# Performance work log

Hardware: AMD Instinct MI355X
Metric: run time of the kernel (lower is better)

## Reference

```python
import jax, jax.numpy as jnp
import numpy as np
import itertools, math

B, T, D = 4, 4096, 1024
H = 16
DIM = D // H          # 64
L, KB = 8, 4
R = 1 << KB           # 16
S = L * R             # 128
TOPK = 2


def setup_inputs() -> dict:
    key = jax.random.key(0)
    ks = jax.random.split(key, 8)
    x = jax.random.normal(ks[0], (B, T, D), dtype=jnp.float32)
    mask = jnp.ones((B, T), dtype=jnp.float32)
    sc = 1.0 / math.sqrt(D)
    Wq = jax.random.normal(ks[1], (D, D), dtype=jnp.float32) * sc
    Wk = jax.random.normal(ks[2], (D, D), dtype=jnp.float32) * sc
    Wv = jax.random.normal(ks[3], (D, D), dtype=jnp.float32) * sc
    Wout = jax.random.normal(ks[4], (D, D), dtype=jnp.float32) * sc
    b_out = jnp.zeros((D,), dtype=jnp.float32)
    # planes: (L, K_bits, head_dim) -> stored transposed as (head_dim, L*K_bits)
    planes = jax.random.normal(ks[5], (L * KB, DIM), dtype=jnp.float32)
    planes_T = planes.T
    # hypercube corners (R, K_bits) -> stored transposed as (K_bits, R)
    corners = jnp.asarray(list(itertools.product([-1.0, 1.0], repeat=KB)), dtype=jnp.float32)
    protos_T = corners.T
    logit_temp = jnp.zeros((), dtype=jnp.float32)  # log(1.0)
    return {"x": x, "mask": mask, "Wq": Wq, "Wk": Wk, "Wv": Wv,
            "Wout": Wout, "b_out": b_out, "planes_T": planes_T,
            "protos_T": protos_T, "logit_temp": logit_temp}


def reference(x, mask, Wq, Wk, Wv, Wout, b_out, planes_T, protos_T, logit_temp):
    b, t, d = x.shape
    Q = (x @ Wq).reshape(b, t, H, DIM)
    K = (x @ Wk).reshape(b, t, H, DIM)
    V = (x @ Wv).reshape(b, t, H, DIM)
    m = mask[:, :, None, None]
    Q, K, V = Q * m, K * m, V * m
    Q = jnp.transpose(Q, (0, 2, 1, 3))  # [B,H,T,dim]
    K = jnp.transpose(K, (0, 2, 1, 3))
    V = jnp.transpose(V, (0, 2, 1, 3))

    scale = jnp.clip(jnp.exp(logit_temp), 0.01, 20.0)
    # LSH hyperplane projections of K
    projK = jnp.einsum('bhtd,dp->bhtp', K, planes_T).reshape(b, H, t, L, KB)
    logitsK = jnp.einsum('bhtlk,kr->bhtlr', jnp.tanh(projK) / scale, protos_T)
    probsK = jax.nn.softmax(logitsK, axis=-1)  # [B,H,T,L,R]

    # top-k mask over R, then renormalize
    _, top_idx = jax.lax.top_k(probsK, TOPK)
    sel = jax.nn.one_hot(top_idx, R, dtype=probsK.dtype).sum(axis=-2)
    probsK = probsK * sel
    probsK = probsK / (probsK.sum(axis=-1, keepdims=True) + 1e-6)

    assign = probsK.reshape(b, H, t, S)  # [B,H,T,S]
    bucket_K = jnp.einsum('bhts,bhtd->bhsd', assign, K)
    bucket_V = jnp.einsum('bhts,bhtd->bhsd', assign, V)
    A = assign.sum(axis=2)[..., None]  # [B,H,S,1]
    bucket_K = bucket_K / (A + 1e-6)
    bucket_V = bucket_V / (A + 1e-6)

    scores = jnp.einsum('bhtd,bhsd->bhts', Q, bucket_K) / math.sqrt(DIM)
    probs_attn = jax.nn.softmax(scores, axis=-1)
    out = jnp.einsum('bhts,bhsd->bhtd', probs_attn, bucket_V)
    out = jnp.transpose(out, (0, 2, 1, 3)).reshape(b, t, d)
    return out @ Wout + b_out
```

## Files before the change

kernel.cpp:

```cpp
#include <hip/hip_runtime.h>
#include <math.h>
#include <stdint.h>

#define TT   4096
#define DD   1024
#define HH   16
#define DIMM 64
#define SS   128

typedef short bf16x8 __attribute__((ext_vector_type(8)));
typedef float f32x4  __attribute__((ext_vector_type(4)));

__device__ __forceinline__ unsigned short f2bf(float f) {
    uint32_t u = __float_as_uint(f);
    return (unsigned short)((u + 0x7fffu + ((u >> 16) & 1u)) >> 16);
}
__device__ __forceinline__ float bf2f(unsigned short h) {
    return __uint_as_float((uint32_t)h << 16);
}

#define GLD16(ldsp, gp) __builtin_amdgcn_global_load_lds( \
    (const __attribute__((address_space(1))) uint32_t*)(gp), \
    (__attribute__((address_space(3))) uint32_t*)(ldsp), 16, 0, 0)

__global__ __launch_bounds__(256) void cvt2_k(const float* __restrict__ x,
                                              unsigned short* __restrict__ xb,
                                              unsigned short* __restrict__ xlo)
{
    const size_t i = ((size_t)blockIdx.x * 256 + threadIdx.x) * 8;
    const float4 a = *(const float4*)&x[i];
    const float4 b = *(const float4*)&x[i + 4];
    const float v[8] = {a.x, a.y, a.z, a.w, b.x, b.y, b.z, b.w};
    unsigned short h[8], l[8];
#pragma unroll
    for (int j = 0; j < 8; j++) {
        h[j] = f2bf(v[j]);
        l[j] = f2bf(v[j] - bf2f(h[j]));
    }
    uint4 rh, rl;
    rh.x = (uint32_t)h[0] | ((uint32_t)h[1] << 16);
    rh.y = (uint32_t)h[2] | ((uint32_t)h[3] << 16);
    rh.z = (uint32_t)h[4] | ((uint32_t)h[5] << 16);
    rh.w = (uint32_t)h[6] | ((uint32_t)h[7] << 16);
    rl.x = (uint32_t)l[0] | ((uint32_t)l[1] << 16);
    rl.y = (uint32_t)l[2] | ((uint32_t)l[3] << 16);
    rl.z = (uint32_t)l[4] | ((uint32_t)l[5] << 16);
    rl.w = (uint32_t)l[6] | ((uint32_t)l[7] << 16);
    *(uint4*)&xb[i]  = rh;
    *(uint4*)&xlo[i] = rl;
}

__global__ __launch_bounds__(256) void tr_k(const float* __restrict__ W,
                                            unsigned short* __restrict__ WT)
{
    __shared__ unsigned short tile[32][33];
    const int bx = blockIdx.x * 32;
    const int by = blockIdx.y * 32;
    const int tx = threadIdx.x & 31, ty = threadIdx.x >> 5;
#pragma unroll
    for (int r = 0; r < 4; r++) {
        const int row = by + ty * 4 + r;
        tile[tx][ty * 4 + r] = f2bf(W[(size_t)row * 1024 + bx + tx]);
    }
    __syncthreads();
#pragma unroll
    for (int r = 0; r < 4; r++) {
        const int col = bx + ty * 4 + r;
        WT[(size_t)col * 1024 + by + tx] = tile[ty * 4 + r][tx];
    }
}

__global__ __launch_bounds__(256) void tr2_k(const float* __restrict__ Wp,
                                             unsigned short* __restrict__ WphT,
                                             unsigned short* __restrict__ WplT)
{
    __shared__ float tile[32][33];
    const int bx = blockIdx.x * 32;
    const int by = blockIdx.y * 32;
    const int tx = threadIdx.x & 31, ty = threadIdx.x >> 5;
#pragma unroll
    for (int r = 0; r < 4; r++) {
        const int row = by + ty * 4 + r;
        tile[tx][ty * 4 + r] = Wp[(size_t)row * 512 + bx + tx];
    }
    __syncthreads();
#pragma unroll
    for (int r = 0; r < 4; r++) {
        const int col = bx + ty * 4 + r;
        const float v = tile[ty * 4 + r][tx];
        const unsigned short hi = f2bf(v);
        const unsigned short lo = f2bf(v - bf2f(hi));
        WphT[(size_t)col * 1024 + by + tx] = hi;
        WplT[(size_t)col * 1024 + by + tx] = lo;
    }
}

template<int MODE>
__global__ __launch_bounds__(256) void mgemm_k(
    const unsigned short* __restrict__ Abf, const unsigned short* __restrict__ BT,
    const float* __restrict__ aux, float* __restrict__ C)
{
    __shared__ short sA[4096];
    __shared__ short sB[4096];
    const int tid = threadIdx.x;
    const int w  = tid >> 6;
    const int ln = tid & 63;
    const int wm = w & 1, wn = w >> 1;
    const int row0 = blockIdx.y * 128;
    const int col0 = blockIdx.x * 128;
    const int lr = ln >> 4, lc = ln & 15;

    f32x4 acc[4][4];
#pragma unroll
    for (int i = 0; i < 4; i++)
#pragma unroll
        for (int j = 0; j < 4; j++) acc[i][j] = (f32x4){0.f, 0.f, 0.f, 0.f};

    const int ia0 = 2 * w, ia1 = 2 * w + 1;
    const size_t gA0 = (size_t)(row0 + ia0 * 16 + lc) * 1024 + lr * 8;
    const size_t gA1 = (size_t)(row0 + ia1 * 16 + lc) * 1024 + lr * 8;
    const size_t gB0 = (size_t)(col0 + ia0 * 16 + lc) * 1024 + lr * 8;
    const size_t gB1 = (size_t)(col0 + ia1 * 16 + lc) * 1024 + lr * 8;

    for (int k0 = 0; k0 < 1024; k0 += 32) {
        GLD16(&sA[ia0 * 512], Abf + gA0 + k0);
        GLD16(&sA[ia1 * 512], Abf + gA1 + k0);
        GLD16(&sB[ia0 * 512], BT  + gB0 + k0);
        GLD16(&sB[ia1 * 512], BT  + gB1 + k0);
        __syncthreads();

        bf16x8 af[4], bfr[4];
#pragma unroll
        for (int ib = 0; ib < 4; ib++)
            af[ib] = *(const bf16x8*)&sA[(wm * 4 + ib) * 512 + ln * 8];
#pragma unroll
        for (int jb = 0; jb < 4; jb++)
            bfr[jb] = *(const bf16x8*)&sB[(wn * 4 + jb) * 512 + ln * 8];
#pragma unroll
        for (int ib = 0; ib < 4; ib++)
#pragma unroll
            for (int jb = 0; jb < 4; jb++)
                acc[ib][jb] = __builtin_amdgcn_mfma_f32_16x16x32_bf16(
                    af[ib], bfr[jb], acc[ib][jb], 0, 0, 0);
        __syncthreads();
    }

    if (MODE == 0) {
        const int h = col0 / 64 + wn;
#pragma unroll
        for (int ib = 0; ib < 4; ib++) {
#pragma unroll
            for (int r = 0; r < 4; r++) {
                const int gr = row0 + wm * 64 + ib * 16 + lr * 4 + r;
                const float mval = aux[gr];
                const int b = gr >> 12, t = gr & (TT - 1);
                float* base = C + (((size_t)(b * HH + h) * TT + t) * DIMM);
#pragma unroll
                for (int jb = 0; jb < 4; jb++)
                    base[jb * 16 + lc] = acc[ib][jb][r] * mval;
            }
        }
    } else if (MODE == 1) {
#pragma unroll
        for (int ib = 0; ib < 4; ib++) {
#pragma unroll
            for (int r = 0; r < 4; r++) {
                const int gr = row0 + wm * 64 + ib * 16 + lr * 4 + r;
#pragma unroll
                for (int jb = 0; jb < 4; jb++) {
                    const int col = col0 + wn * 64 + jb * 16 + lc;
                    C[(size_t)gr * 1024 + col] = acc[ib][jb][r] + aux[col];
                }
            }
        }
    } else {
        const int h = col0 / 64 + wn;
        unsigned short* Qf = (unsigned short*)C;
#pragma unroll
        for (int ib = 0; ib < 4; ib++) {
#pragma unroll
            for (int r = 0; r < 4; r++) {
                const int gr = row0 + wm * 64 + ib * 16 + lr * 4 + r;
                const float mval = aux[gr];
                const int b = gr >> 12;
                const int tt = gr & 127;
                const size_t tbase = (size_t)(b * HH + h) * 262144
                                   + (size_t)((gr & (TT - 1)) >> 7) * 8192;
#pragma unroll
                for (int jb = 0; jb < 4; jb++) {
                    const int d = jb * 16 + lc;
                    const int e = ((tt >> 4) * 2 + (d >> 5)) * 512 +
                                  ((tt & 15) + ((d >> 3) & 3) * 16) * 8 + (d & 7);
                    Qf[tbase + e] = f2bf(acc[ib][jb][r] * mval);
                }
            }
        }
    }
}

__global__ __launch_bounds__(256) void projm_k(
    const unsigned short* __restrict__ Ah, const unsigned short* __restrict__ Al,
    const unsigned short* __restrict__ Bh, const unsigned short* __restrict__ Bl,
    const float* __restrict__ mask, float* __restrict__ P)
{
    __shared__ short sAh[4096];
    __shared__ short sAl[4096];
    __shared__ short sBh[4096];
    __shared__ short sBl[4096];
    const int tid = threadIdx.x;
    const int w  = tid >> 6;
    const int ln = tid & 63;
    const int wm = w & 1, wn = w >> 1;
    const int row0 = blockIdx.y * 128;
    const int col0 = blockIdx.x * 128;
    const int lr = ln >> 4, lc = ln & 15;

    f32x4 acc[4][4];
#pragma unroll
    for (int i = 0; i < 4; i++)
#pragma unroll
        for (int j = 0; j < 4; j++) acc[i][j] = (f32x4){0.f, 0.f, 0.f, 0.f};

    const int ia0 = 2 * w, ia1 = 2 * w + 1;
    const size_t gA0 = (size_t)(row0 + ia0 * 16 + lc) * 1024 + lr * 8;
    const size_t gA1 = (size_t)(row0 + ia1 * 16 + lc) * 1024 + lr * 8;
    const size_t gB0 = (size_t)(col0 + ia0 * 16 + lc) * 1024 + lr * 8;
    const size_t gB1 = (size_t)(col0 + ia1 * 16 + lc) * 1024 + lr * 8;

    for (int k0 = 0; k0 < 1024; k0 += 32) {
        GLD16(&sAh[ia0 * 512], Ah + gA0 + k0);
        GLD16(&sAh[ia1 * 512], Ah + gA1 + k0);
        GLD16(&sAl[ia0 * 512], Al + gA0 + k0);
        GLD16(&sAl[ia1 * 512], Al + gA1 + k0);
        GLD16(&sBh[ia0 * 512], Bh + gB0 + k0);
        GLD16(&sBh[ia1 * 512], Bh + gB1 + k0);
        GLD16(&sBl[ia0 * 512], Bl + gB0 + k0);
        GLD16(&sBl[ia1 * 512], Bl + gB1 + k0);
        __syncthreads();

        bf16x8 ah[4], al[4], bh[4], bl[4];
#pragma unroll
        for (int ib = 0; ib < 4; ib++) {
            ah[ib] = *(const bf16x8*)&sAh[(wm * 4 + ib) * 512 + ln * 8];
            al[ib] = *(const bf16x8*)&sAl[(wm * 4 + ib) * 512 + ln * 8];
        }
#pragma unroll
        for (int jb = 0; jb < 4; jb++) {
            bh[jb] = *(const bf16x8*)&sBh[(wn * 4 + jb) * 512 + ln * 8];
            bl[jb] = *(const bf16x8*)&sBl[(wn * 4 + jb) * 512 + ln * 8];
        }
#pragma unroll
        for (int ib = 0; ib < 4; ib++)
#pragma unroll
            for (int jb = 0; jb < 4; jb++) {
                acc[ib][jb] = __builtin_amdgcn_mfma_f32_16x16x32_bf16(
                    ah[ib], bh[jb], acc[ib][jb], 0, 0, 0);
                acc[ib][jb] = __builtin_amdgcn_mfma_f32_16x16x32_bf16(
                    ah[ib], bl[jb], acc[ib][jb], 0, 0, 0);
                acc[ib][jb] = __builtin_amdgcn_mfma_f32_16x16x32_bf16(
                    al[ib], bh[jb], acc[ib][jb], 0, 0, 0);
            }
        __syncthreads();
    }

#pragma unroll
    for (int ib = 0; ib < 4; ib++) {
#pragma unroll
        for (int r = 0; r < 4; r++) {
            const int gr = row0 + wm * 64 + ib * 16 + lr * 4 + r;
            const float mval = mask[gr];
            const int b = gr >> 12, t = gr & (TT - 1);
#pragma unroll
            for (int jb = 0; jb < 4; jb++) {
                const int c = col0 + wn * 64 + jb * 16 + lc;
                const int h = c >> 5, p = c & 31;
                P[(((size_t)(b * HH + h) * TT + t) * 32) + p] =
                    acc[ib][jb][r] * mval;
            }
        }
    }
}

__global__ __launch_bounds__(256) void wproj_k(
    const float* __restrict__ Wk, const float* __restrict__ planesT,
    float* __restrict__ Wp)
{
    __shared__ float sW[1024];
    __shared__ float sP[2048];
    const int tid = threadIdx.x;
    const int k = blockIdx.x;
    for (int i = tid; i < 1024; i += 256) sW[i] = Wk[(size_t)k * 1024 + i];
    for (int i = tid; i < 2048; i += 256) sP[i] = planesT[i];
    __syncthreads();
#pragma unroll
    for (int c0 = 0; c0 < 2; c0++) {
        const int c = c0 * 256 + tid;
        const int h = c >> 5, p = c & 31;
        float s = 0.f;
#pragma unroll
        for (int d = 0; d < 64; d++)
            s = fmaf(sW[h * 64 + d], sP[d * 32 + p], s);
        Wp[(size_t)k * 512 + c] = s;
    }
}

__global__ __launch_bounds__(256) void zero_k(float* __restrict__ p)
{
    const size_t i = ((size_t)blockIdx.x * 256 + threadIdx.x) * 4;
    *(float4*)&p[i] = make_float4(0.f, 0.f, 0.f, 0.f);
}

__global__ __launch_bounds__(256) void assign_k(
    const float* __restrict__ Pj, const float* __restrict__ protosT,
    const float* __restrict__ logit_temp,
    unsigned char* __restrict__ aIdx, float* __restrict__ aW,
    float* __restrict__ gA)
{
    __shared__ float sPr[4][16];
    __shared__ float sCnt[SS];
    const int tid = threadIdx.x;
    const int tc = blockIdx.x;
    const int bh = blockIdx.y;

    if (tid < 64)  ((float*)sPr)[tid] = protosT[tid];
    if (tid < SS)  sCnt[tid] = 0.f;
    __syncthreads();

    const float scale = fminf(fmaxf(__expf(logit_temp[0]), 0.01f), 20.0f);
    const float inv_scale = 1.0f / scale;

    const int t = tc * 256 + tid;
    const float* pr = Pj + ((size_t)bh * TT + t) * 32;
    float proj[32];
#pragma unroll
    for (int j = 0; j < 8; j++) {
        const float4 v = *(const float4*)&pr[j * 4];
        proj[j * 4 + 0] = v.x; proj[j * 4 + 1] = v.y;
        proj[j * 4 + 2] = v.z; proj[j * 4 + 3] = v.w;
    }
#pragma unroll
    for (int p = 0; p < 32; p++) proj[p] = tanhf(proj[p]) * inv_scale;

    unsigned char idx[16];
    float wv[16];
#pragma unroll
    for (int l = 0; l < 8; l++) {
        float g[16];
#pragma unroll
        for (int r = 0; r < 16; r++)
            g[r] = proj[l * 4 + 0] * sPr[0][r] + proj[l * 4 + 1] * sPr[1][r] +
                   proj[l * 4 + 2] * sPr[2][r] + proj[l * 4 + 3] * sPr[3][r];
        float mx = g[0];
#pragma unroll
        for (int r = 1; r < 16; r++) mx = fmaxf(mx, g[r]);
        float Zs = 0.f;
#pragma unroll
        for (int r = 0; r < 16; r++) Zs += __expf(g[r] - mx);
        int a = 0; float ga = g[0];
#pragma unroll
        for (int r = 1; r < 16; r++) { if (g[r] > ga) { ga = g[r]; a = r; } }
        int b2 = (a == 0) ? 1 : 0; float gb = g[b2];
#pragma unroll
        for (int r = 0; r < 16; r++) { if (r != a && g[r] > gb) { gb = g[r]; b2 = r; } }
        const float pa = __expf(ga - mx) / Zs;
        const float pb = __expf(gb - mx) / Zs;
        const float den = pa + pb + 1e-6f;
        const float wa = pa / den, wb = pb / den;
        idx[l * 2 + 0] = (unsigned char)(l * 16 + a);  wv[l * 2 + 0] = wa;
        idx[l * 2 + 1] = (unsigned char)(l * 16 + b2); wv[l * 2 + 1] = wb;
        atomicAdd(&sCnt[l * 16 + a],  wa);
        atomicAdd(&sCnt[l * 16 + b2], wb);
    }
    const size_t off = (size_t)bh * TT + t;
    uint32_t pk[4];
#pragma unroll
    for (int j = 0; j < 4; j++)
        pk[j] = (uint32_t)idx[j * 4] | ((uint32_t)idx[j * 4 + 1] << 8) |
                ((uint32_t)idx[j * 4 + 2] << 16) | ((uint32_t)idx[j * 4 + 3] << 24);
    *(uint4*)&aIdx[off * 16] = make_uint4(pk[0], pk[1], pk[2], pk[3]);
#pragma unroll
    for (int j = 0; j < 4; j++)
        *(float4*)&aW[off * 16 + j * 4] =
            make_float4(wv[j * 4], wv[j * 4 + 1], wv[j * 4 + 2], wv[j * 4 + 3]);
    __syncthreads();
    if (tid < SS) atomicAdd(&gA[bh * SS + tid], sCnt[tid]);
}

__global__ __launch_bounds__(256) void scatter4_k(
    const float* __restrict__ Kb, const float* __restrict__ Vb,
    const unsigned char* __restrict__ aIdx, const float* __restrict__ aW,
    float* __restrict__ gBK, float* __restrict__ gBV)
{
    __shared__ short sA[8192];
    __shared__ short sB[8192];
    const int tid = threadIdx.x;
    const int tc = blockIdx.x;
    const int bh = blockIdx.y;
    const int w  = tid >> 6, ln = tid & 63;
    const int wm = w & 1, wn = w >> 1;

    f32x4 acc[4][4];
#pragma unroll
    for (int i = 0; i < 4; i++)
#pragma unroll
        for (int j = 0; j < 4; j++) acc[i][j] = (f32x4){0.f, 0.f, 0.f, 0.f};

    const int scol = tid & 127;
    const int stg  = tid >> 7;
    const float* srcrow = (scol < 64)
        ? Kb + (size_t)bh * (TT * DIMM) + scol
        : Vb + (size_t)bh * (TT * DIMM) + (scol - 64);
    const int bchunk = (scol >> 4);
    const int bslot8 = (scol & 15) * 8;
    const int ptt = tid >> 2, pg = tid & 3;

    for (int c = 0; c < 8; c++) {
        const int t0 = tc * 512 + c * 64;
        __syncthreads();
        {
            const uint4 z = make_uint4(0u, 0u, 0u, 0u);
#pragma unroll
            for (int r = 0; r < 4; r++)
                *(uint4*)&sA[(r * 256 + tid) * 8] = z;
        }
        __syncthreads();
#pragma unroll 8
        for (int r = 0; r < 32; r++) {
            const int tt = stg * 32 + r;
            const float v = srcrow[(size_t)(t0 + tt) * DIMM];
            sB[((tt >> 5) * 8 + bchunk) * 512 + ((tt >> 3) & 3) * 128 +
               bslot8 + (tt & 7)] = f2bf(v);
        }
        {
            const size_t off = (size_t)bh * TT + (t0 + ptt);
            const uint32_t pk = ((const uint32_t*)aIdx)[off * 4 + pg];
            const float4 wv = *(const float4*)&aW[off * 16 + pg * 4];
            const float w4[4] = {wv.x, wv.y, wv.z, wv.w};
#pragma unroll
            for (int q = 0; q < 4; q++) {
                const int s = (pk >> (8 * q)) & 255;
                sA[((ptt >> 5) * 8 + (s >> 4)) * 512 + ((ptt >> 3) & 3) * 128 +
                   (s & 15) * 8 + (ptt & 7)] = f2bf(w4[q]);
            }
        }
        __syncthreads();
#pragma unroll
        for (int ks = 0; ks < 2; ks++) {
            bf16x8 af[4], bfr[4];
#pragma unroll
            for (int ib = 0; ib < 4; ib++)
                af[ib] = *(const bf16x8*)&sA[(ks * 8 + wm * 4 + ib) * 512 + ln * 8];
#pragma unroll
            for (int jb = 0; jb < 4; jb++)
                bfr[jb] = *(const bf16x8*)&sB[(ks * 8 + wn * 4 + jb) * 512 + ln * 8];
#pragma unroll
            for (int ib = 0; ib < 4; ib++)
#pragma unroll
                for (int jb = 0; jb < 4; jb++)
                    acc[ib][jb] = __builtin_amdgcn_mfma_f32_16x16x32_bf16(
                        af[ib], bfr[jb], acc[ib][jb], 0, 0, 0);
        }
    }

    const int lr = ln >> 4, lc = ln & 15;
#pragma unroll
    for (int ib = 0; ib < 4; ib++) {
#pragma unroll
        for (int r = 0; r < 4; r++) {
            const int s = wm * 64 + ib * 16 + lr * 4 + r;
#pragma unroll
            for (int jb = 0; jb < 4; jb++) {
                const int col = wn * 64 + jb * 16 + lc;
                if (col < 64)
                    atomicAdd(&gBK[(size_t)bh * (SS * DIMM) + s * DIMM + col],
                              acc[ib][jb][r]);
                else
                    atomicAdd(&gBV[(size_t)bh * (SS * DIMM) + s * DIMM + (col - 64)],
                              acc[ib][jb][r]);
            }
        }
    }
}

__global__ __launch_bounds__(256) void bprep_k(
    const float* __restrict__ gBK, const float* __restrict__ gBV,
    const float* __restrict__ gA,
    unsigned short* __restrict__ Kf, unsigned short* __restrict__ VTf)
{
    __shared__ float sInv[SS];
    const int tid = threadIdx.x;
    const int bh = blockIdx.y;
    if (tid < SS) sInv[tid] = 1.0f / (gA[bh * SS + tid] + 1e-6f);
    __syncthreads();
#pragma unroll
    for (int it = 0; it < 8; it++) {
        const int i = (blockIdx.x * 8 + it) * 256 + tid;
        const int s = i >> 6, d = i & 63;
        const float kv = gBK[(size_t)bh * 8192 + i] * sInv[s];
        const float vv = gBV[(size_t)bh * 8192 + i] * sInv[s];
        const int ek = ((s >> 4) * 2 + (d >> 5)) * 512 +
                       ((s & 15) + ((d >> 3) & 3) * 16) * 8 + (d & 7);
        const int ev = ((d >> 4) * 4 + (s >> 5)) * 512 +
                       ((d & 15) + ((s >> 3) & 3) * 16) * 8 + (s & 7);
        Kf[(size_t)bh * 8192 + ek]  = f2bf(kv);
        VTf[(size_t)bh * 8192 + ev] = f2bf(vv);
    }
}

__global__ __launch_bounds__(256) void attn_m(
    const unsigned short* __restrict__ Qf, const unsigned short* __restrict__ Kf,
    const unsigned short* __restrict__ VTf, unsigned short* __restrict__ attb)
{
    __shared__ short sQ[8192];
    __shared__ short sK[8192];
    __shared__ short sVT[8192];
    __shared__ short sP[16384];
    const int tid = threadIdx.x;
    const int tc = blockIdx.x;
    const int bh = blockIdx.y;
    const int w = tid >> 6, l = tid & 63;

    const size_t qbase  = (size_t)bh * 262144 + (size_t)tc * 8192;
    const size_t kvbase = (size_t)bh * 8192;
#pragma unroll
    for (int i = 0; i < 4; i++) {
        const int o = (i * 256 + w * 64) * 8;
        GLD16(&sQ[o],  Qf  + qbase  + o + l * 8);
        GLD16(&sK[o],  Kf  + kvbase + o + l * 8);
        GLD16(&sVT[o], VTf + kvbase + o + l * 8);
    }
    __syncthreads();

    f32x4 acc[2][8];
#pragma unroll
    for (int i = 0; i < 2; i++)
#pragma unroll
        for (int j = 0; j < 8; j++) acc[i][j] = (f32x4){0.f, 0.f, 0.f, 0.f};

#pragma unroll
    for (int ks = 0; ks < 2; ks++) {
        const bf16x8 a0 = *(const bf16x8*)&sQ[((w * 2 + 0) * 2 + ks) * 512 + l * 8];
        const bf16x8 a1 = *(const bf16x8*)&sQ[((w * 2 + 1) * 2 + ks) * 512 + l * 8];
#pragma unroll
        for (int jb = 0; jb < 8; jb++) {
            const bf16x8 b = *(const bf16x8*)&sK[(jb * 2 + ks) * 512 + l * 8];
            acc[0][jb] = __builtin_amdgcn_mfma_f32_16x16x32_bf16(a0, b, acc[0][jb], 0, 0, 0);
            acc[1][jb] = __builtin_amdgcn_mfma_f32_16x16x32_bf16(a1, b, acc[1][jb], 0, 0, 0);
        }
    }

#pragma unroll
    for (int ib = 0; ib < 2; ib++) {
        const int mb = w * 2 + ib;
#pragma unroll
        for (int r = 0; r < 4; r++) {
            float v[8];
            float mx = -INFINITY;
#pragma unroll
            for (int jb = 0; jb < 8; jb++) {
                v[jb] = acc[ib][jb][r] * 0.125f;
                mx = fmaxf(mx, v[jb]);
            }
            mx = fmaxf(mx, __shfl_xor(mx, 1));
            mx = fmaxf(mx, __shfl_xor(mx, 2));
            mx = fmaxf(mx, __shfl_xor(mx, 4));
            mx = fmaxf(mx, __shfl_xor(mx, 8));
            float Z = 0.f;
#pragma unroll
            for (int jb = 0; jb < 8; jb++) { v[jb] = __expf(v[jb] - mx); Z += v[jb]; }
            Z += __shfl_xor(Z, 1);
            Z += __shfl_xor(Z, 2);
            Z += __shfl_xor(Z, 4);
            Z += __shfl_xor(Z, 8);
            const float invZ = 1.0f / Z;
            const int ttl = (l >> 4) * 4 + r;
#pragma unroll
            for (int jb = 0; jb < 8; jb++) {
                int e = (mb * 4 + (jb >> 1)) * 512 +
                        (ttl + (((jb * 2 + ((l >> 3) & 1)) & 3) * 16)) * 8 + (l & 7);
                e ^= ((e >> 7) & 3) << 4;
                sP[e] = (short)f2bf(v[jb] * invZ);
            }
        }
    }

    f32x4 acc2[2][4];
#pragma unroll
    for (int i = 0; i < 2; i++)
#pragma unroll
        for (int j = 0; j < 4; j++) acc2[i][j] = (f32x4){0.f, 0.f, 0.f, 0.f};

#pragma unroll
    for (int ks = 0; ks < 4; ks++) {
        bf16x8 a[2];
#pragma unroll
        for (int ib = 0; ib < 2; ib++) {
            int ia = ((w * 2 + ib) * 4 + ks) * 512 + l * 8;
            ia ^= ((ia >> 7) & 3) << 4;
            a[ib] = *(const bf16x8*)&sP[ia];
        }
#pragma unroll
        for (int jb = 0; jb < 4; jb++) {
            const bf16x8 b = *(const bf16x8*)&sVT[(jb * 4 + ks) * 512 + l * 8];
            acc2[0][jb] = __builtin_amdgcn_mfma_f32_16x16x32_bf16(a[0], b, acc2[0][jb], 0, 0, 0);
            acc2[1][jb] = __builtin_amdgcn_mfma_f32_16x16x32_bf16(a[1], b, acc2[1][jb], 0, 0, 0);
        }
    }

    const int b = bh >> 4, h = bh & 15;
#pragma unroll
    for (int ib = 0; ib < 2; ib++) {
#pragma unroll
        for (int r = 0; r < 4; r++) {
            const int t = tc * 128 + w * 32 + ib * 16 + (l >> 4) * 4 + r;
            unsigned short* outp = attb + ((size_t)(b * TT + t)) * DD + h * DIMM;
#pragma unroll
            for (int jb = 0; jb < 4; jb++)
                outp[jb * 16 + (l & 15)] = f2bf(acc2[ib][jb][r]);
        }
    }
}

extern "C" void kernel_launch(void* const* d_in, const int* in_sizes, int n_in,
                              void* d_out, int out_size, void* d_ws, size_t ws_size,
                              hipStream_t stream)
{
    const float* x       = (const float*)d_in[0];
    const float* mask    = (const float*)d_in[1];
    const float* Wq      = (const float*)d_in[2];
    const float* Wk      = (const float*)d_in[3];
    const float* Wv      = (const float*)d_in[4];
    const float* Wout    = (const float*)d_in[5];
    const float* b_out   = (const float*)d_in[6];
    const float* planesT = (const float*)d_in[7];
    const float* protosT = (const float*)d_in[8];
    const float* ltemp   = (const float*)d_in[9];
    float* out = (float*)d_out;

    float* ws  = (float*)d_ws;
    float* Kb  = ws + (1u << 24);
    float* Vb  = ws + (2u << 24);
    float* gBK = ws + (3u << 24);
    float* gBV = gBK + 524288;
    float* gA  = gBV + 524288;
    unsigned short* Qf    = (unsigned short*)ws;
    unsigned short* WT1   = (unsigned short*)gBK;
    unsigned short* WvT   = (unsigned short*)gBV;
    unsigned short* xb    = (unsigned short*)(ws + 51388416);
    unsigned short* xlo   = (unsigned short*)Vb;
    float*          Wp    = ws;
    unsigned short* WphT  = (unsigned short*)(ws + 524288);
    unsigned short* WplT  = (unsigned short*)(ws + 786432);
    float*          aW    = ws + 51388416;
    unsigned char*  aIdx  = (unsigned char*)(ws + 55582720);
    unsigned short* Kf    = (unsigned short*)(ws + 56631296);
    unsigned short* VTf   = (unsigned short*)(ws + 56893440);
    unsigned short* attb  = (unsigned short*)Vb;
    unsigned short* WoutT = (unsigned short*)(ws + 41943040);
    float*          Pj    = (float*)d_out;

    const dim3 mg(8, 128);
    const dim3 tg(32, 32);
    const dim3 t2g(16, 32);
    const dim3 pg(4, 128);

    cvt2_k<<<8192, 256, 0, stream>>>(x, xb, xlo);

    wproj_k<<<1024, 256, 0, stream>>>(Wk, planesT, Wp);
    tr2_k<<<t2g, 256, 0, stream>>>(Wp, WphT, WplT);
    projm_k<<<pg, 256, 0, stream>>>(xb, xlo, WphT, WplT, mask, Pj);

    tr_k<<<tg, 256, 0, stream>>>(Wq, WT1);
    mgemm_k<2><<<mg, 256, 0, stream>>>(xb, WT1, mask, (float*)Qf);
    tr_k<<<tg, 256, 0, stream>>>(Wk, WT1);
    mgemm_k<0><<<mg, 256, 0, stream>>>(xb, WT1, mask, Kb);
    tr_k<<<tg, 256, 0, stream>>>(Wv, WvT);
    mgemm_k<0><<<mg, 256, 0, stream>>>(xb, WvT, mask, Vb);

    zero_k<<<1032, 256, 0, stream>>>(gBK);
    assign_k<<<dim3(16, 64), 256, 0, stream>>>(Pj, protosT, ltemp, aIdx, aW, gA);
    scatter4_k<<<dim3(8, 64), 256, 0, stream>>>(Kb, Vb, aIdx, aW, gBK, gBV);

    bprep_k<<<dim3(4, 64), 256, 0, stream>>>(gBK, gBV, gA, Kf, VTf);
    tr_k<<<tg, 256, 0, stream>>>(Wout, WoutT);
    attn_m<<<dim3(32, 64), 256, 0, stream>>>(Qf, Kf, VTf, attb);

    mgemm_k<1><<<mg, 256, 0, stream>>>(attb, WoutT, b_out, out);
}
```

Baseline: 686.0 us.

## Fuse QKV projections into one GEMM with double-buffered LDS and XCD-aware block mapping

Merges the three separate Q, K and V GEMM launches into a single kernel over a concatenated transposed weight buffer, with the epilogue choosing the output format by column block. All GEMM kernels (QKV, output, projection) now double-buffer their LDS tiles so global-to-LDS loads for the next K-slice overlap MFMA work on the current one. Blocks are remapped so that consecutive row bands land on the same XCD, aiming for better L2 reuse of the A operand. Double buffering doubles LDS use per block, which may lower occupancy, especially for projm_k with four operand buffers. The QKV GEMM also reads the next stage's global-to-LDS loads without an explicit wait before the single barrier, relying on __syncthreads to cover it.

```diff
diff --git a/kernel.cpp b/kernel.cpp
--- a/kernel.cpp
+++ b/kernel.cpp
@@ -95,19 +95,23 @@
     }
 }
 
-template<int MODE>
-__global__ __launch_bounds__(256) void mgemm_k(
+__global__ __launch_bounds__(256) void qkv_k(
     const unsigned short* __restrict__ Abf, const unsigned short* __restrict__ BT,
-    const float* __restrict__ aux, float* __restrict__ C)
-{
-    __shared__ short sA[4096];
-    __shared__ short sB[4096];
+    const float* __restrict__ mask, unsigned short* __restrict__ Qf,
+    float* __restrict__ Kb, float* __restrict__ Vb)
+{
+    __shared__ short sA[2][4096];
+    __shared__ short sB[2][4096];
     const int tid = threadIdx.x;
     const int w  = tid >> 6;
     const int ln = tid & 63;
     const int wm = w & 1, wn = w >> 1;
-    const int row0 = blockIdx.y * 128;
-    const int col0 = blockIdx.x * 128;
+    const int id   = blockIdx.y * 24 + blockIdx.x;
+    const int xcd  = id & 7, kk = id >> 3;
+    const int band = xcd * 16 + kk / 24;
+    const int colblk = kk % 24;
+    const int row0 = band * 128;
+    const int col0 = colblk * 128;
     const int lr = ln >> 4, lc = ln & 15;
 
     f32x4 acc[4][4];
@@ -122,20 +126,25 @@
     const size_t gB0 = (size_t)(col0 + ia0 * 16 + lc) * 1024 + lr * 8;
     const size_t gB1 = (size_t)(col0 + ia1 * 16 + lc) * 1024 + lr * 8;
 
-    for (int k0 = 0; k0 < 1024; k0 += 32) {
-        GLD16(&sA[ia0 * 512], Abf + gA0 + k0);
-        GLD16(&sA[ia1 * 512], Abf + gA1 + k0);
-        GLD16(&sB[ia0 * 512], BT  + gB0 + k0);
-        GLD16(&sB[ia1 * 512], BT  + gB1 + k0);
-        __syncthreads();
-
+    auto STAGE = [&](int buf, int k0) {
+        GLD16(&sA[buf][ia0 * 512], Abf + gA0 + k0);
+        GLD16(&sA[buf][ia1 * 512], Abf + gA1 + k0);
+        GLD16(&sB[buf][ia0 * 512], BT  + gB0 + k0);
+        GLD16(&sB[buf][ia1 * 512], BT  + gB1 + k0);
+    };
+
+    STAGE(0, 0);
+    __syncthreads();
+    for (int t = 0; t < 32; t++) {
+        const int cur = t & 1;
+        if (t < 31) STAGE(cur ^ 1, (t + 1) * 32);
         bf16x8 af[4], bfr[4];
 #pragma unroll
         for (int ib = 0; ib < 4; ib++)
-            af[ib] = *(const bf16x8*)&sA[(wm * 4 + ib) * 512 + ln * 8];
+            af[ib] = *(const bf16x8*)&sA[cur][(wm * 4 + ib) * 512 + ln * 8];
 #pragma unroll
         for (int jb = 0; jb < 4; jb++)
-            bfr[jb] = *(const bf16x8*)&sB[(wn * 4 + jb) * 512 + ln * 8];
+            bfr[jb] = *(const bf16x8*)&sB[cur][(wn * 4 + jb) * 512 + ln * 8];
 #pragma unroll
         for (int ib = 0; ib < 4; ib++)
 #pragma unroll
@@ -145,43 +154,16 @@
         __syncthreads();
     }
 
-    if (MODE == 0) {
-        const int h = col0 / 64 + wn;
+    const int proj = colblk >> 3;
+    const int c0l  = (colblk & 7) * 128;
+    const int h    = c0l / 64 + wn;
+    if (proj == 0) {
 #pragma unroll
         for (int ib = 0; ib < 4; ib++) {
 #pragma unroll
             for (int r = 0; r < 4; r++) {
                 const int gr = row0 + wm * 64 + ib * 16 + lr * 4 + r;
-                const float mval = aux[gr];
-                const int b = gr >> 12, t = gr & (TT - 1);
-                float* base = C + (((size_t)(b * HH + h) * TT + t) * DIMM);
-#pragma unroll
-                for (int jb = 0; jb < 4; jb++)
-                    base[jb * 16 + lc] = acc[ib][jb][r] * mval;
-            }
-        }
-    } else if (MODE == 1) {
-#pragma unroll
-        for (int ib = 0; ib < 4; ib++) {
-#pragma unroll
-            for (int r = 0; r < 4; r++) {
-                const int gr = row0 + wm * 64 + ib * 16 + lr * 4 + r;
-#pragma unroll
-                for (int jb = 0; jb < 4; jb++) {
-                    const int col = col0 + wn * 64 + jb * 16 + lc;
-                    C[(size_t)gr * 1024 + col] = acc[ib][jb][r] + aux[col];
-                }
-            }
-        }
-    } else {
-        const int h = col0 / 64 + wn;
-        unsigned short* Qf = (unsigned short*)C;
-#pragma unroll
-        for (int ib = 0; ib < 4; ib++) {
-#pragma unroll
-            for (int r = 0; r < 4; r++) {
-                const int gr = row0 + wm * 64 + ib * 16 + lr * 4 + r;
-                const float mval = aux[gr];
+                const float mval = mask[gr];
                 const int b = gr >> 12;
                 const int tt = gr & 127;
                 const size_t tbase = (size_t)(b * HH + h) * 262144
@@ -195,24 +177,37 @@
                 }
             }
         }
-    }
-}
-
-__global__ __launch_bounds__(256) void projm_k(
-    const unsigned short* __restrict__ Ah, const unsigned short* __restrict__ Al,
-    const unsigned short* __restrict__ Bh, const unsigned short* __restrict__ Bl,
-    const float* __restrict__ mask, float* __restrict__ P)
-{
-    __shared__ short sAh[4096];
-    __shared__ short sAl[4096];
-    __shared__ short sBh[4096];
-    __shared__ short sBl[4096];
+    } else {
+        float* C = (proj == 1) ? Kb : Vb;
+#pragma unroll
+        for (int ib = 0; ib < 4; ib++) {
+#pragma unroll
+            for (int r = 0; r < 4; r++) {
+                const int gr = row0 + wm * 64 + ib * 16 + lr * 4 + r;
+                const float mval = mask[gr];
+                const int b = gr >> 12, t = gr & (TT - 1);
+                float* base = C + (((size_t)(b * HH + h) * TT + t) * DIMM);
+#pragma unroll
+                for (int jb = 0; jb < 4; jb++)
+                    base[jb * 16 + lc] = acc[ib][jb][r] * mval;
+            }
+        }
+    }
+}
+
+__global__ __launch_bounds__(256) void out_k(
+    const unsigned short* __restrict__ Abf, const unsigned short* __restrict__ BT,
+    const float* __restrict__ bias, float* __restrict__ C)
+{
+    __shared__ short sA[2][4096];
+    __shared__ short sB[2][4096];
     const int tid = threadIdx.x;
-    const int w  = tid >> 6;
-    const int ln = tid & 63;
+    const int w  = tid >> 6, ln = tid & 63;
     const int wm = w & 1, wn = w >> 1;
-    const int row0 = blockIdx.y * 128;
-    const int col0 = blockIdx.x * 128;
+    const int id  = blockIdx.y * 8 + blockIdx.x;
+    const int xcd = id & 7, kk = id >> 3;
+    const int row0 = (xcd * 16 + (kk >> 3)) * 128;
+    const int col0 = (kk & 7) * 128;
     const int lr = ln >> 4, lc = ln & 15;
 
     f32x4 acc[4][4];
@@ -227,27 +222,105 @@
     const size_t gB0 = (size_t)(col0 + ia0 * 16 + lc) * 1024 + lr * 8;
     const size_t gB1 = (size_t)(col0 + ia1 * 16 + lc) * 1024 + lr * 8;
 
-    for (int k0 = 0; k0 < 1024; k0 += 32) {
-        GLD16(&sAh[ia0 * 512], Ah + gA0 + k0);
-        GLD16(&sAh[ia1 * 512], Ah + gA1 + k0);
-        GLD16(&sAl[ia0 * 512], Al + gA0 + k0);
-        GLD16(&sAl[ia1 * 512], Al + gA1 + k0);
-        GLD16(&sBh[ia0 * 512], Bh + gB0 + k0);
-        GLD16(&sBh[ia1 * 512], Bh + gB1 + k0);
-        GLD16(&sBl[ia0 * 512], Bl + gB0 + k0);
-        GLD16(&sBl[ia1 * 512], Bl + gB1 + k0);
+    auto STAGE = [&](int buf, int k0) {
+        GLD16(&sA[buf][ia0 * 512], Abf + gA0 + k0);
+        GLD16(&sA[buf][ia1 * 512], Abf + gA1 + k0);
+        GLD16(&sB[buf][ia0 * 512], BT  + gB0 + k0);
+        GLD16(&sB[buf][ia1 * 512], BT  + gB1 + k0);
+    };
+
+    STAGE(0, 0);
+    __syncthreads();
+    for (int t = 0; t < 32; t++) {
+        const int cur = t & 1;
+        if (t < 31) STAGE(cur ^ 1, (t + 1) * 32);
+        bf16x8 af[4], bfr[4];
+#pragma unroll
+        for (int ib = 0; ib < 4; ib++)
+            af[ib] = *(const bf16x8*)&sA[cur][(wm * 4 + ib) * 512 + ln * 8];
+#pragma unroll
+        for (int jb = 0; jb < 4; jb++)
+            bfr[jb] = *(const bf16x8*)&sB[cur][(wn * 4 + jb) * 512 + ln * 8];
+#pragma unroll
+        for (int ib = 0; ib < 4; ib++)
+#pragma unroll
+            for (int jb = 0; jb < 4; jb++)
+                acc[ib][jb] = __builtin_amdgcn_mfma_f32_16x16x32_bf16(
+                    af[ib], bfr[jb], acc[ib][jb], 0, 0, 0);
         __syncthreads();
-
+    }
+
+#pragma unroll
+    for (int ib = 0; ib < 4; ib++) {
+#pragma unroll
+        for (int r = 0; r < 4; r++) {
+            const int gr = row0 + wm * 64 + ib * 16 + lr * 4 + r;
+#pragma unroll
+            for (int jb = 0; jb < 4; jb++) {
+                const int col = col0 + wn * 64 + jb * 16 + lc;
+                C[(size_t)gr * 1024 + col] = acc[ib][jb][r] + bias[col];
+            }
+        }
+    }
+}
+
+__global__ __launch_bounds__(256) void projm_k(
+    const unsigned short* __restrict__ Ah, const unsigned short* __restrict__ Al,
+    const unsigned short* __restrict__ Bh, const unsigned short* __restrict__ Bl,
+    const float* __restrict__ mask, float* __restrict__ P)
+{
+    __shared__ short sAh[2][4096];
+    __shared__ short sAl[2][4096];
+    __shared__ short sBh[2][4096];
+    __shared__ short sBl[2][4096];
+    const int tid = threadIdx.x;
+    const int w  = tid >> 6;
+    const int ln = tid & 63;
+    const int wm = w & 1, wn = w >> 1;
+    const int id  = blockIdx.y * 4 + blockIdx.x;
+    const int xcd = id & 7, kk = id >> 3;
+    const int row0 = (xcd * 16 + (kk >> 2)) * 128;
+    const int col0 = (kk & 3) * 128;
+    const int lr = ln >> 4, lc = ln & 15;
+
+    f32x4 acc[4][4];
+#pragma unroll
+    for (int i = 0; i < 4; i++)
+#pragma unroll
+        for (int j = 0; j < 4; j++) acc[i][j] = (f32x4){0.f, 0.f, 0.f, 0.f};
+
+    const int ia0 = 2 * w, ia1 = 2 * w + 1;
+    const size_t gA0 = (size_t)(row0 + ia0 * 16 + lc) * 1024 + lr * 8;
+    const size_t gA1 = (size_t)(row0 + ia1 * 16 + lc) * 1024 + lr * 8;
+    const size_t gB0 = (size_t)(col0 + ia0 * 16 + lc) * 1024 + lr * 8;
+    const size_t gB1 = (size_t)(col0 + ia1 * 16 + lc) * 1024 + lr * 8;
+
+    auto STAGE = [&](int buf, int k0) {
+        GLD16(&sAh[buf][ia0 * 512], Ah + gA0 + k0);
+        GLD16(&sAh[buf][ia1 * 512], Ah + gA1 + k0);
+        GLD16(&sAl[buf][ia0 * 512], Al + gA0 + k0);
+        GLD16(&sAl[buf][ia1 * 512], Al + gA1 + k0);
+        GLD16(&sBh[buf][ia0 * 512], Bh + gB0 + k0);
+        GLD16(&sBh[buf][ia1 * 512], Bh + gB1 + k0);
+        GLD16(&sBl[buf][ia0 * 512], Bl + gB0 + k0);
+        GLD16(&sBl[buf][ia1 * 512], Bl + gB1 + k0);
+    };
+
+    STAGE(0, 0);
+    __syncthreads();
+    for (int t = 0; t < 32; t++) {
+        const int cur = t & 1;
+        if (t < 31) STAGE(cur ^ 1, (t + 1) * 32);
         bf16x8 ah[4], al[4], bh[4], bl[4];
 #pragma unroll
         for (int ib = 0; ib < 4; ib++) {
-            ah[ib] = *(const bf16x8*)&sAh[(wm * 4 + ib) * 512 + ln * 8];
-            al[ib] = *(const bf16x8*)&sAl[(wm * 4 + ib) * 512 + ln * 8];
+            ah[ib] = *(const bf16x8*)&sAh[cur][(wm * 4 + ib) * 512 + ln * 8];
+            al[ib] = *(const bf16x8*)&sAl[cur][(wm * 4 + ib) * 512 + ln * 8];
         }
 #pragma unroll
         for (int jb = 0; jb < 4; jb++) {
-            bh[jb] = *(const bf16x8*)&sBh[(wn * 4 + jb) * 512 + ln * 8];
-            bl[jb] = *(const bf16x8*)&sBl[(wn * 4 + jb) * 512 + ln * 8];
+            bh[jb] = *(const bf16x8*)&sBh[cur][(wn * 4 + jb) * 512 + ln * 8];
+            bl[jb] = *(const bf16x8*)&sBl[cur][(wn * 4 + jb) * 512 + ln * 8];
         }
 #pragma unroll
         for (int ib = 0; ib < 4; ib++)
@@ -644,8 +717,6 @@
     float* gBV = gBK + 524288;
     float* gA  = gBV + 524288;
     unsigned short* Qf    = (unsigned short*)ws;
-    unsigned short* WT1   = (unsigned short*)gBK;
-    unsigned short* WvT   = (unsigned short*)gBV;
     unsigned short* xb    = (unsigned short*)(ws + 51388416);
     unsigned short* xlo   = (unsigned short*)Vb;
     float*          Wp    = ws;
@@ -658,11 +729,13 @@
     unsigned short* attb  = (unsigned short*)Vb;
     unsigned short* WoutT = (unsigned short*)(ws + 41943040);
     float*          Pj    = (float*)d_out;
-
-    const dim3 mg(8, 128);
+    unsigned short* BTall = (unsigned short*)((float*)d_out + 8388608);
+
     const dim3 tg(32, 32);
     const dim3 t2g(16, 32);
     const dim3 pg(4, 128);
+    const dim3 qg(24, 128);
+    const dim3 og(8, 128);
 
     cvt2_k<<<8192, 256, 0, stream>>>(x, xb, xlo);
 
@@ -670,12 +743,10 @@
     tr2_k<<<t2g, 256, 0, stream>>>(Wp, WphT, WplT);
     projm_k<<<pg, 256, 0, stream>>>(xb, xlo, WphT, WplT, mask, Pj);
 
-    tr_k<<<tg, 256, 0, stream>>>(Wq, WT1);
-    mgemm_k<2><<<mg, 256, 0, stream>>>(xb, WT1, mask, (float*)Qf);
-    tr_k<<<tg, 256, 0, stream>>>(Wk, WT1);
-    mgemm_k<0><<<mg, 256, 0, stream>>>(xb, WT1, mask, Kb);
-    tr_k<<<tg, 256, 0, stream>>>(Wv, WvT);
-    mgemm_k<0><<<mg, 256, 0, stream>>>(xb, WvT, mask, Vb);
+    tr_k<<<tg, 256, 0, stream>>>(Wq, BTall);
+    tr_k<<<tg, 256, 0, stream>>>(Wk, BTall + 1048576);
+    tr_k<<<tg, 256, 0, stream>>>(Wv, BTall + 2097152);
+    qkv_k<<<qg, 256, 0, stream>>>(xb, BTall, mask, Qf, Kb, Vb);
 
     zero_k<<<1032, 256, 0, stream>>>(gBK);
     assign_k<<<dim3(16, 64), 256, 0, stream>>>(Pj, protosT, ltemp, aIdx, aW, gA);
@@ -685,5 +756,5 @@
     tr_k<<<tg, 256, 0, stream>>>(Wout, WoutT);
     attn_m<<<dim3(32, 64), 256, 0, stream>>>(Qf, Kf, VTf, attb);
 
-    mgemm_k<1><<<mg, 256, 0, stream>>>(attb, WoutT, b_out, out);
-}
+    out_k<<<og, 256, 0, stream>>>(attb, WoutT, b_out, out);
+}
```

New measurement: 659.9 us. -3.8%, faster.
